# Optimization experiments

Hardware: AMD Instinct MI355X
Metric: run time of the kernel (lower is better)

The kernel has to match this reference:

```python
import jax, jax.numpy as jnp
import numpy as np

D_MODEL = 1024
N_HEAD = 16
D_K = D_MODEL // N_HEAD
B, S = 2, 2048
NEG = -1000000000.0


def setup_inputs() -> dict:
    key = jax.random.key(0)
    ks = jax.random.split(key, 9)
    inp = {
        "input_q": jax.random.normal(ks[0], (B, S, D_MODEL), dtype=jnp.float32),
        "input_k": jax.random.normal(ks[1], (B, S, D_MODEL), dtype=jnp.float32),
        "input_v": jax.random.normal(ks[2], (B, S, D_MODEL), dtype=jnp.float32),
        "mask": jax.random.randint(ks[3], (1, 1, S, S), 0, 2, dtype=jnp.int32),
        # parameters (Linear weights stored as [in, out] for x @ W)
        "w_q": jax.random.normal(ks[4], (D_MODEL, D_MODEL), dtype=jnp.float32) / np.sqrt(D_MODEL),
        "w_k": jax.random.normal(ks[5], (D_MODEL, D_MODEL), dtype=jnp.float32) / np.sqrt(D_MODEL),
        "w_v": jax.random.normal(ks[6], (D_MODEL, D_MODEL), dtype=jnp.float32) / np.sqrt(D_MODEL),
        "w_o": jax.random.normal(ks[7], (D_MODEL, D_MODEL), dtype=jnp.float32) / np.sqrt(D_MODEL),
        "b_o": jax.random.normal(ks[8], (D_MODEL,), dtype=jnp.float32) * 0.01,
    }
    return inp


def reference(input_q, input_k, input_v, mask, w_q, w_k, w_v, w_o, b_o):
    b = input_q.shape[0]
    # QKV projections -> [B, H, S, d_k]
    def split_heads(x):
        return x.reshape(b, -1, N_HEAD, D_K).transpose(0, 2, 1, 3)
    q = split_heads(input_q @ w_q)
    k = split_heads(input_k @ w_k)
    v = split_heads(input_v @ w_v)
    # naive attention: materialize [B, H, Sq, Sk] scores
    scores = jnp.einsum("bhqd,bhkd->bhqk", q, k) / jnp.sqrt(jnp.float32(D_K))
    scores = jnp.where(mask == 0, jnp.float32(NEG), scores)
    attn = jax.nn.softmax(scores, axis=-1)
    per_head = jnp.einsum("bhqk,bhkd->bhqd", attn, v)
    concat = per_head.transpose(0, 2, 1, 3).reshape(b, -1, N_HEAD * D_K)
    return concat @ w_o + b_o
```

## Files before the change

### kernel.cpp

```cpp
#include <hip/hip_runtime.h>
#include <hip/hip_bf16.h>

typedef _Float16 halfx8 __attribute__((ext_vector_type(8)));
typedef _Float16 halfx4 __attribute__((ext_vector_type(4)));
typedef _Float16 half2t __attribute__((ext_vector_type(2)));
typedef __fp16 fp16x2 __attribute__((ext_vector_type(2)));
typedef float floatx4 __attribute__((ext_vector_type(4)));

constexpr int S = 2048;
constexpr int DM = 1024;
constexpr int NH = 16;
constexpr int DK = 64;
constexpr int BATCH = 2;
constexpr int MROWS = 4096;
constexpr float QSCALE = 0.125f * 1.44269504088896340736f;

#if defined(__has_builtin)
#if __has_builtin(__builtin_amdgcn_fdot2)
#define HAVE_FDOT2 1
#endif
#endif

static __device__ inline half2t pack2(float a, float b) {
  return __builtin_bit_cast(half2t, __builtin_amdgcn_cvt_pkrtz(a, b));
}

__global__ void convert_w4(const float* __restrict__ w0, const float* __restrict__ w1,
                           const float* __restrict__ w2, const float* __restrict__ w3,
                           _Float16* __restrict__ o0, _Float16* __restrict__ o1,
                           _Float16* __restrict__ o2, _Float16* __restrict__ o3) {
  const float* w = (blockIdx.z == 0) ? w0 : (blockIdx.z == 1) ? w1 : (blockIdx.z == 2) ? w2 : w3;
  _Float16* wt = (blockIdx.z == 0) ? o0 : (blockIdx.z == 1) ? o1 : (blockIdx.z == 2) ? o2 : o3;
  __shared__ float tile[32][33];
  int n0 = blockIdx.x * 32, k0 = blockIdx.y * 32;
  int tx = threadIdx.x, ty = threadIdx.y;
#pragma unroll
  for (int i = 0; i < 4; ++i)
    tile[ty + i * 8][tx] = w[(k0 + ty + i * 8) * DM + n0 + tx];
  __syncthreads();
#pragma unroll
  for (int i = 0; i < 4; ++i)
    wt[(n0 + ty + i * 8) * DM + k0 + tx] = (_Float16)tile[tx][ty + i * 8];
}

__global__ void convert_in3(const float* __restrict__ a0, const float* __restrict__ a1,
                            const float* __restrict__ a2, _Float16* __restrict__ o0,
                            _Float16* __restrict__ o1, _Float16* __restrict__ o2) {
  const float* a = (blockIdx.z == 0) ? a0 : (blockIdx.z == 1) ? a1 : a2;
  _Float16* o = (blockIdx.z == 0) ? o0 : (blockIdx.z == 1) ? o1 : o2;
  size_t i = ((size_t)blockIdx.x * 256 + threadIdx.x) * 8;
  float4 va = *(const float4*)(a + i);
  float4 vb = *(const float4*)(a + i + 4);
  union { halfx8 v; _Float16 h[8]; } u;
  u.h[0] = (_Float16)va.x; u.h[1] = (_Float16)va.y;
  u.h[2] = (_Float16)va.z; u.h[3] = (_Float16)va.w;
  u.h[4] = (_Float16)vb.x; u.h[5] = (_Float16)vb.y;
  u.h[6] = (_Float16)vb.z; u.h[7] = (_Float16)vb.w;
  *(halfx8*)(o + i) = u.v;
}

__global__ void mask_fp16(const int* __restrict__ m, _Float16* __restrict__ Mh) {
  size_t i = ((size_t)blockIdx.x * 256 + threadIdx.x) * 8;
  int4 a = *(const int4*)(m + i);
  int4 b = *(const int4*)(m + i + 4);
  union { halfx8 v; _Float16 h[8]; } u;
  u.h[0] = (_Float16)(a.x != 0); u.h[1] = (_Float16)(a.y != 0);
  u.h[2] = (_Float16)(a.z != 0); u.h[3] = (_Float16)(a.w != 0);
  u.h[4] = (_Float16)(b.x != 0); u.h[5] = (_Float16)(b.y != 0);
  u.h[6] = (_Float16)(b.z != 0); u.h[7] = (_Float16)(b.w != 0);
  *(halfx8*)(Mh + i) = u.v;
}

__global__ __launch_bounds__(256) void qkv_gemm(const _Float16* __restrict__ xq,
                                                const _Float16* __restrict__ xk,
                                                const _Float16* __restrict__ xv,
                                                const _Float16* __restrict__ wqkv,
                                                _Float16* __restrict__ Qh,
                                                _Float16* __restrict__ Kh,
                                                _Float16* __restrict__ Vt) {
  constexpr int LDT = 72;
  __shared__ __align__(16) _Float16 smem[2 * 128 * LDT];
  _Float16* Asm = smem;
  _Float16* Bsm = smem + 128 * LDT;
  const int tid = threadIdx.x;
  const int w = tid >> 6, l = tid & 63, lo = l & 15, quad = l >> 4;
  const int wm = (w >> 1) * 64, wn = (w & 1) * 64;
  const int bx = blockIdx.x, bm = blockIdx.y * 128;
  const int wid = bx >> 3;
  const _Float16* A = (wid == 0) ? xq : (wid == 1) ? xk : xv;
  const _Float16* Bt = wqkv + (size_t)bx * 128 * DM;

  const int srow = tid >> 1, scol = (tid & 1) * 32;
  const _Float16* Aptr = A + (size_t)(bm + srow) * DM + scol;
  const _Float16* Bptr = Bt + (size_t)srow * DM + scol;

  floatx4 acc[4][4] = {};

  for (int k0 = 0; k0 < DM; k0 += 64) {
#pragma unroll
    for (int i = 0; i < 4; ++i)
      *(halfx8*)&Asm[srow * LDT + scol + i * 8] = *(const halfx8*)(Aptr + k0 + i * 8);
#pragma unroll
    for (int i = 0; i < 4; ++i)
      *(halfx8*)&Bsm[srow * LDT + scol + i * 8] = *(const halfx8*)(Bptr + k0 + i * 8);
    __syncthreads();

#pragma unroll
    for (int ks = 0; ks < 2; ++ks) {
      halfx8 af[4], bf[4];
#pragma unroll
      for (int mt = 0; mt < 4; ++mt)
        af[mt] = *(const halfx8*)&Asm[(wm + mt * 16 + lo) * LDT + ks * 32 + quad * 8];
#pragma unroll
      for (int nt = 0; nt < 4; ++nt)
        bf[nt] = *(const halfx8*)&Bsm[(wn + nt * 16 + lo) * LDT + ks * 32 + quad * 8];
#pragma unroll
      for (int mt = 0; mt < 4; ++mt)
#pragma unroll
        for (int nt = 0; nt < 4; ++nt)
          acc[mt][nt] =
              __builtin_amdgcn_mfma_f32_16x16x32_f16(af[mt], bf[nt], acc[mt][nt], 0, 0, 0);
    }
    __syncthreads();
  }

  if (wid == 2) {
    constexpr int LDTT = 136;
    _Float16* tb = smem;
#pragma unroll
    for (int mt = 0; mt < 4; ++mt)
#pragma unroll
      for (int nt = 0; nt < 4; ++nt)
#pragma unroll
        for (int r = 0; r < 4; ++r) {
          int dl = wn + nt * 16 + lo;
          int sl = wm + mt * 16 + quad * 4 + r;
          tb[dl * LDTT + sl] = (_Float16)acc[mt][nt][r];
        }
    __syncthreads();
    const int b = bm >> 11, s0 = bm & (S - 1);
    const int d2 = tid >> 1, chunk = (tid & 1) * 64;
    const int dg = ((bx & 7) * 128 + d2);
    const int h = dg >> 6, dd = dg & 63;
    _Float16* O = Vt + ((size_t)(b * NH + h) * DK + dd) * S + s0 + chunk;
#pragma unroll
    for (int j = 0; j < 8; ++j)
      *(halfx8*)(O + j * 8) = *(const halfx8*)&tb[d2 * LDTT + chunk + j * 8];
    return;
  }

  _Float16* Out = (wid == 0) ? Qh : Kh;
  const float scale = (wid == 0) ? QSCALE : 1.0f;
#pragma unroll
  for (int mt = 0; mt < 4; ++mt)
#pragma unroll
    for (int nt = 0; nt < 4; ++nt)
#pragma unroll
      for (int r = 0; r < 4; ++r) {
        int row = bm + wm + mt * 16 + quad * 4 + r;
        int n = (bx & 7) * 128 + wn + nt * 16 + lo;
        int b = row >> 11, s = row & (S - 1);
        int h = n >> 6, d = n & 63;
        Out[((size_t)(b * NH + h) * S + s) * DK + d] = (_Float16)(acc[mt][nt][r] * scale);
      }
}

__global__ __launch_bounds__(256) void attn_kernel(const _Float16* __restrict__ Q,
                                                   const _Float16* __restrict__ Kh,
                                                   const _Float16* __restrict__ Vt,
                                                   const _Float16* __restrict__ Mh,
                                                   _Float16* __restrict__ concat) {
  constexpr int LDT = 72;
  __shared__ __align__(16) _Float16 Ksm[64 * LDT];
  __shared__ __align__(16) _Float16 Vsm[64 * LDT];
  __shared__ __align__(16) _Float16 Psm[4 * 16 * LDT];

  const int tid = threadIdx.x;
  const int w = tid >> 6, l = tid & 63, lo = l & 15, quad = l >> 4;
  const int qb = blockIdx.x * 64 + w * 16;
  const int h = blockIdx.y, b = blockIdx.z;

  const _Float16* Qb = Q + (size_t)(b * NH + h) * S * DK;
  const _Float16* Kb = Kh + (size_t)(b * NH + h) * S * DK;
  const _Float16* Vb = Vt + (size_t)(b * NH + h) * DK * S;
  const _Float16* Mq = Mh + (size_t)(qb + lo) * S;

  halfx8 qf[2];
#pragma unroll
  for (int ks = 0; ks < 2; ++ks)
    qf[ks] = *(const halfx8*)(Qb + (qb + lo) * DK + ks * 32 + quad * 8);

  floatx4 Oacc[4] = {};
  float lsum = 0.f;
  const half2t onev = {(_Float16)1.0f, (_Float16)1.0f};

  const int srow = tid >> 2, scol = (tid & 3) * 16;
  const _Float16* Kp = Kb + srow * DK + scol;
  const _Float16* Vp = Vb + srow * S + scol;
  _Float16* Pw = &Psm[w * 16 * LDT];

  for (int kt = 0; kt < S / 64; ++kt) {
#pragma unroll
    for (int i = 0; i < 2; ++i) {
      *(halfx8*)&Ksm[srow * LDT + scol + i * 8] = *(const halfx8*)(Kp + kt * 64 * DK + i * 8);
      *(halfx8*)&Vsm[srow * LDT + scol + i * 8] = *(const halfx8*)(Vp + kt * 64 + i * 8);
    }
    __syncthreads();

    floatx4 Sacc[4] = {};
#pragma unroll
    for (int ks = 0; ks < 2; ++ks)
#pragma unroll
      for (int nt = 0; nt < 4; ++nt) {
        halfx8 kf = *(const halfx8*)&Ksm[(nt * 16 + lo) * LDT + ks * 32 + quad * 8];
        Sacc[nt] = __builtin_amdgcn_mfma_f32_16x16x32_f16(kf, qf[ks], Sacc[nt], 0, 0, 0);
      }

#pragma unroll
    for (int nt = 0; nt < 4; ++nt) {
      union { halfx4 v; half2t h[2]; } mv;
      mv.v = *(const halfx4*)(Mq + kt * 64 + nt * 16 + quad * 4);
      half2t p01 = pack2(__builtin_exp2f(Sacc[nt][0]), __builtin_exp2f(Sacc[nt][1]));
      half2t p23 = pack2(__builtin_exp2f(Sacc[nt][2]), __builtin_exp2f(Sacc[nt][3]));
      p01 *= mv.h[0];
      p23 *= mv.h[1];
#ifdef HAVE_FDOT2
      lsum = __builtin_amdgcn_fdot2(__builtin_bit_cast(fp16x2, p01),
                                    __builtin_bit_cast(fp16x2, onev), lsum, false);
      lsum = __builtin_amdgcn_fdot2(__builtin_bit_cast(fp16x2, p23),
                                    __builtin_bit_cast(fp16x2, onev), lsum, false);
#else
      lsum += (float)p01[0] + (float)p01[1] + (float)p23[0] + (float)p23[1];
#endif
      union { halfx4 v; half2t h[2]; } u;
      u.h[0] = p01; u.h[1] = p23;
      *(halfx4*)&Pw[lo * LDT + nt * 16 + quad * 4] = u.v;
    }

#pragma unroll
    for (int ks = 0; ks < 2; ++ks) {
      halfx8 pf = *(const halfx8*)&Pw[lo * LDT + ks * 32 + quad * 8];
#pragma unroll
      for (int nt = 0; nt < 4; ++nt) {
        halfx8 vf = *(const halfx8*)&Vsm[(nt * 16 + lo) * LDT + ks * 32 + quad * 8];
        Oacc[nt] = __builtin_amdgcn_mfma_f32_16x16x32_f16(pf, vf, Oacc[nt], 0, 0, 0);
      }
    }
    __syncthreads();
  }

  lsum += __shfl_xor(lsum, 16);
  lsum += __shfl_xor(lsum, 32);

#pragma unroll
  for (int r = 0; r < 4; ++r) {
    float lr = __shfl(lsum, quad * 4 + r);
    float inv = __builtin_amdgcn_rcpf(lr);
    int q = qb + quad * 4 + r;
#pragma unroll
    for (int nt = 0; nt < 4; ++nt) {
      int d = nt * 16 + lo;
      concat[((size_t)b * S + q) * DM + h * DK + d] = (_Float16)(Oacc[nt][r] * inv);
    }
  }
}

__global__ __launch_bounds__(256) void out_gemm(const _Float16* __restrict__ A,
                                                const _Float16* __restrict__ Bt,
                                                float* __restrict__ Cp,
                                                const float* __restrict__ bias) {
  constexpr int LDT = 72;
  __shared__ __align__(16) _Float16 Asm[128 * LDT];
  __shared__ __align__(16) _Float16 Bsm[64 * LDT];
  const int tid = threadIdx.x;
  const int w = tid >> 6, l = tid & 63, lo = l & 15, quad = l >> 4;
  const int wm = (w >> 1) * 64, wn = (w & 1) * 32;
  const int bm = blockIdx.y * 128, bn = blockIdx.x * 64;

  const int arow = tid >> 1, acol = (tid & 1) * 32;
  const int brow = tid >> 2, bcol = (tid & 3) * 16;

  floatx4 acc[4][2] = {};

  for (int k0 = 0; k0 < DM; k0 += 64) {
#pragma unroll
    for (int i = 0; i < 4; ++i)
      *(halfx8*)&Asm[arow * LDT + acol + i * 8] =
          *(const halfx8*)(A + (size_t)(bm + arow) * DM + k0 + acol + i * 8);
#pragma unroll
    for (int i = 0; i < 2; ++i)
      *(halfx8*)&Bsm[brow * LDT + bcol + i * 8] =
          *(const halfx8*)(Bt + (size_t)(bn + brow) * DM + k0 + bcol + i * 8);
    __syncthreads();

#pragma unroll
    for (int ks = 0; ks < 2; ++ks) {
      halfx8 af[4], bfr[2];
#pragma unroll
      for (int mt = 0; mt < 4; ++mt)
        af[mt] = *(const halfx8*)&Asm[(wm + mt * 16 + lo) * LDT + ks * 32 + quad * 8];
#pragma unroll
      for (int nt = 0; nt < 2; ++nt)
        bfr[nt] = *(const halfx8*)&Bsm[(wn + nt * 16 + lo) * LDT + ks * 32 + quad * 8];
#pragma unroll
      for (int mt = 0; mt < 4; ++mt)
#pragma unroll
        for (int nt = 0; nt < 2; ++nt)
          acc[mt][nt] =
              __builtin_amdgcn_mfma_f32_16x16x32_f16(af[mt], bfr[nt], acc[mt][nt], 0, 0, 0);
    }
    __syncthreads();
  }

#pragma unroll
  for (int mt = 0; mt < 4; ++mt)
#pragma unroll
    for (int nt = 0; nt < 2; ++nt)
#pragma unroll
      for (int r = 0; r < 4; ++r) {
        int row = bm + wm + mt * 16 + quad * 4 + r;
        int col = bn + wn + nt * 16 + lo;
        Cp[(size_t)row * DM + col] = acc[mt][nt][r] + bias[col];
      }
}

extern "C" void kernel_launch(void* const* d_in, const int* in_sizes, int n_in,
                              void* d_out, int out_size, void* d_ws, size_t ws_size,
                              hipStream_t stream) {
  const float* in_q = (const float*)d_in[0];
  const float* in_k = (const float*)d_in[1];
  const float* in_v = (const float*)d_in[2];
  const int* mask = (const int*)d_in[3];
  const float* w_q = (const float*)d_in[4];
  const float* w_k = (const float*)d_in[5];
  const float* w_v = (const float*)d_in[6];
  const float* w_o = (const float*)d_in[7];
  const float* b_o = (const float*)d_in[8];
  float* out = (float*)d_out;

  char* ws = (char*)d_ws;
  constexpr size_t WB = (size_t)DM * DM * sizeof(_Float16);
  constexpr size_t MB_ = (size_t)S * S * sizeof(_Float16);
  constexpr size_t TB = (size_t)MROWS * DM * sizeof(_Float16);
  _Float16* wqkv = (_Float16*)(ws);
  _Float16* wto = (_Float16*)(ws + 3 * WB);
  _Float16* Mh = (_Float16*)(ws + 4 * WB);
  char* p = ws + 4 * WB + MB_;
  _Float16* Qh = (_Float16*)(p);
  _Float16* Kh = (_Float16*)(p + TB);
  _Float16* Vt = (_Float16*)(p + 2 * TB);
  _Float16* xq = (_Float16*)(p + 3 * TB);
  _Float16* xk = (_Float16*)(p + 4 * TB);
  _Float16* xv = (_Float16*)(p + 5 * TB);
  _Float16* concat = xq;

  convert_w4<<<dim3(32, 32, 4), dim3(32, 8), 0, stream>>>(
      w_q, w_k, w_v, w_o, wqkv, wqkv + DM * DM, wqkv + 2 * DM * DM, wto);
  convert_in3<<<dim3(MROWS * DM / 8 / 256, 1, 3), 256, 0, stream>>>(in_q, in_k, in_v,
                                                                    xq, xk, xv);
  mask_fp16<<<dim3(S * S / 8 / 256), 256, 0, stream>>>(mask, Mh);

  qkv_gemm<<<dim3(24, 32), 256, 0, stream>>>(xq, xk, xv, wqkv, Qh, Kh, Vt);
  attn_kernel<<<dim3(S / 64, NH, BATCH), 256, 0, stream>>>(Qh, Kh, Vt, Mh, concat);
  out_gemm<<<dim3(DM / 64, MROWS / 128), 256, 0, stream>>>(concat, wto, out, b_o);
}
```

Measured before the change: 293.7 us.

## Use direct global-to-LDS loads with XOR-swizzled tiles and pre-swizzled mask layout

All three matmul-style kernels now stage tiles with global_load_lds (16-byte direct-to-LDS loads) into unpadded 64-wide tiles that use an XOR swizzle to avoid bank conflicts, in place of register round-trips into padded LDS. Q and K are stored row-major as [B*S, DM] instead of per-head layouts, which simplifies the GEMM epilogue. The mask is pre-rearranged into a per-tile, per-lane order so each lane fetches its 16 mask values with two 16-byte loads issued before the barrier. This reduces VGPR traffic and load latency, at the cost of a more complex addressing scheme and reliance on the direct-LDS builtin's placement semantics.

```diff
diff --git a/kernel.cpp b/kernel.cpp
--- a/kernel.cpp
+++ b/kernel.cpp
@@ -23,6 +23,11 @@
 
 static __device__ inline half2t pack2(float a, float b) {
   return __builtin_bit_cast(half2t, __builtin_amdgcn_cvt_pkrtz(a, b));
+}
+
+static __device__ inline void load_lds16(const _Float16* g, _Float16* l) {
+  __builtin_amdgcn_global_load_lds((const __attribute__((address_space(1))) void*)g,
+                                   (__attribute__((address_space(3))) void*)l, 16, 0, 0);
 }
 
 __global__ void convert_w4(const float* __restrict__ w0, const float* __restrict__ w1,
@@ -59,50 +64,59 @@
   *(halfx8*)(o + i) = u.v;
 }
 
-__global__ void mask_fp16(const int* __restrict__ m, _Float16* __restrict__ Mh) {
-  size_t i = ((size_t)blockIdx.x * 256 + threadIdx.x) * 8;
-  int4 a = *(const int4*)(m + i);
-  int4 b = *(const int4*)(m + i + 4);
+__global__ void mask_swz(const int* __restrict__ m, _Float16* __restrict__ Mt) {
+  int t = blockIdx.x * 256 + threadIdx.x;
+  int j0 = (t & 1) * 8;
+  int quad = (t >> 1) & 3;
+  int q = (t >> 3) & (S - 1);
+  int kt = t >> 14;
+  const int* src = m + (size_t)q * S + kt * 64 + (j0 >> 2) * 16 + quad * 4;
+  int4 a = *(const int4*)src;
+  int4 b = *(const int4*)(src + 16);
   union { halfx8 v; _Float16 h[8]; } u;
   u.h[0] = (_Float16)(a.x != 0); u.h[1] = (_Float16)(a.y != 0);
   u.h[2] = (_Float16)(a.z != 0); u.h[3] = (_Float16)(a.w != 0);
   u.h[4] = (_Float16)(b.x != 0); u.h[5] = (_Float16)(b.y != 0);
   u.h[6] = (_Float16)(b.z != 0); u.h[7] = (_Float16)(b.w != 0);
-  *(halfx8*)(Mh + i) = u.v;
+  *(halfx8*)(Mt + (size_t)t * 8) = u.v;
 }
 
 __global__ __launch_bounds__(256) void qkv_gemm(const _Float16* __restrict__ xq,
                                                 const _Float16* __restrict__ xk,
                                                 const _Float16* __restrict__ xv,
                                                 const _Float16* __restrict__ wqkv,
-                                                _Float16* __restrict__ Qh,
-                                                _Float16* __restrict__ Kh,
+                                                _Float16* __restrict__ Qf,
+                                                _Float16* __restrict__ Kf,
                                                 _Float16* __restrict__ Vt) {
-  constexpr int LDT = 72;
-  __shared__ __align__(16) _Float16 smem[2 * 128 * LDT];
+  __shared__ __align__(16) _Float16 smem[17408];
   _Float16* Asm = smem;
-  _Float16* Bsm = smem + 128 * LDT;
+  _Float16* Bsm = smem + 128 * 64;
   const int tid = threadIdx.x;
   const int w = tid >> 6, l = tid & 63, lo = l & 15, quad = l >> 4;
+  const int lo7 = l & 7;
   const int wm = (w >> 1) * 64, wn = (w & 1) * 64;
   const int bx = blockIdx.x, bm = blockIdx.y * 128;
   const int wid = bx >> 3;
   const _Float16* A = (wid == 0) ? xq : (wid == 1) ? xk : xv;
   const _Float16* Bt = wqkv + (size_t)bx * 128 * DM;
 
-  const int srow = tid >> 1, scol = (tid & 1) * 32;
-  const _Float16* Aptr = A + (size_t)(bm + srow) * DM + scol;
-  const _Float16* Bptr = Bt + (size_t)srow * DM + scol;
-
   floatx4 acc[4][4] = {};
 
   for (int k0 = 0; k0 < DM; k0 += 64) {
 #pragma unroll
-    for (int i = 0; i < 4; ++i)
-      *(halfx8*)&Asm[srow * LDT + scol + i * 8] = *(const halfx8*)(Aptr + k0 + i * 8);
-#pragma unroll
-    for (int i = 0; i < 4; ++i)
-      *(halfx8*)&Bsm[srow * LDT + scol + i * 8] = *(const halfx8*)(Bptr + k0 + i * 8);
+    for (int i = 0; i < 4; ++i) {
+      int chunk = i * 256 + tid;
+      int r = chunk >> 3;
+      int c = (chunk & 7) ^ (r & 7);
+      load_lds16(A + (size_t)(bm + r) * DM + k0 + c * 8, Asm + chunk * 8);
+    }
+#pragma unroll
+    for (int i = 0; i < 4; ++i) {
+      int chunk = i * 256 + tid;
+      int r = chunk >> 3;
+      int c = (chunk & 7) ^ (r & 7);
+      load_lds16(Bt + (size_t)r * DM + k0 + c * 8, Bsm + chunk * 8);
+    }
     __syncthreads();
 
 #pragma unroll
@@ -110,10 +124,10 @@
       halfx8 af[4], bf[4];
 #pragma unroll
       for (int mt = 0; mt < 4; ++mt)
-        af[mt] = *(const halfx8*)&Asm[(wm + mt * 16 + lo) * LDT + ks * 32 + quad * 8];
+        af[mt] = *(const halfx8*)&Asm[(wm + mt * 16 + lo) * 64 + (((ks * 4 + quad) ^ lo7) * 8)];
 #pragma unroll
       for (int nt = 0; nt < 4; ++nt)
-        bf[nt] = *(const halfx8*)&Bsm[(wn + nt * 16 + lo) * LDT + ks * 32 + quad * 8];
+        bf[nt] = *(const halfx8*)&Bsm[(wn + nt * 16 + lo) * 64 + (((ks * 4 + quad) ^ lo7) * 8)];
 #pragma unroll
       for (int mt = 0; mt < 4; ++mt)
 #pragma unroll
@@ -149,7 +163,7 @@
     return;
   }
 
-  _Float16* Out = (wid == 0) ? Qh : Kh;
+  _Float16* Out = (wid == 0) ? Qf : Kf;
   const float scale = (wid == 0) ? QSCALE : 1.0f;
 #pragma unroll
   for (int mt = 0; mt < 4; ++mt)
@@ -158,53 +172,51 @@
 #pragma unroll
       for (int r = 0; r < 4; ++r) {
         int row = bm + wm + mt * 16 + quad * 4 + r;
-        int n = (bx & 7) * 128 + wn + nt * 16 + lo;
-        int b = row >> 11, s = row & (S - 1);
-        int h = n >> 6, d = n & 63;
-        Out[((size_t)(b * NH + h) * S + s) * DK + d] = (_Float16)(acc[mt][nt][r] * scale);
+        int col = (bx & 7) * 128 + wn + nt * 16 + lo;
+        Out[(size_t)row * DM + col] = (_Float16)(acc[mt][nt][r] * scale);
       }
 }
 
-__global__ __launch_bounds__(256) void attn_kernel(const _Float16* __restrict__ Q,
-                                                   const _Float16* __restrict__ Kh,
+__global__ __launch_bounds__(256) void attn_kernel(const _Float16* __restrict__ Qf,
+                                                   const _Float16* __restrict__ Kf,
                                                    const _Float16* __restrict__ Vt,
-                                                   const _Float16* __restrict__ Mh,
+                                                   const _Float16* __restrict__ Mt,
                                                    _Float16* __restrict__ concat) {
-  constexpr int LDT = 72;
-  __shared__ __align__(16) _Float16 Ksm[64 * LDT];
-  __shared__ __align__(16) _Float16 Vsm[64 * LDT];
-  __shared__ __align__(16) _Float16 Psm[4 * 16 * LDT];
+  __shared__ __align__(16) _Float16 Ksm[64 * 64];
+  __shared__ __align__(16) _Float16 Vsm[64 * 64];
+  __shared__ __align__(16) _Float16 Psm[4 * 16 * 64];
 
   const int tid = threadIdx.x;
   const int w = tid >> 6, l = tid & 63, lo = l & 15, quad = l >> 4;
+  const int lo7 = l & 7;
   const int qb = blockIdx.x * 64 + w * 16;
   const int h = blockIdx.y, b = blockIdx.z;
 
-  const _Float16* Qb = Q + (size_t)(b * NH + h) * S * DK;
-  const _Float16* Kb = Kh + (size_t)(b * NH + h) * S * DK;
   const _Float16* Vb = Vt + (size_t)(b * NH + h) * DK * S;
-  const _Float16* Mq = Mh + (size_t)(qb + lo) * S;
+  const _Float16* Mw = Mt + ((size_t)(qb + lo) * 4 + quad) * 16;
 
   halfx8 qf[2];
 #pragma unroll
   for (int ks = 0; ks < 2; ++ks)
-    qf[ks] = *(const halfx8*)(Qb + (qb + lo) * DK + ks * 32 + quad * 8);
+    qf[ks] = *(const halfx8*)(Qf + ((size_t)b * S + qb + lo) * DM + h * DK + ks * 32 + quad * 8);
 
   floatx4 Oacc[4] = {};
   float lsum = 0.f;
   const half2t onev = {(_Float16)1.0f, (_Float16)1.0f};
-
-  const int srow = tid >> 2, scol = (tid & 3) * 16;
-  const _Float16* Kp = Kb + srow * DK + scol;
-  const _Float16* Vp = Vb + srow * S + scol;
-  _Float16* Pw = &Psm[w * 16 * LDT];
+  _Float16* Pw = &Psm[w * 16 * 64];
 
   for (int kt = 0; kt < S / 64; ++kt) {
 #pragma unroll
     for (int i = 0; i < 2; ++i) {
-      *(halfx8*)&Ksm[srow * LDT + scol + i * 8] = *(const halfx8*)(Kp + kt * 64 * DK + i * 8);
-      *(halfx8*)&Vsm[srow * LDT + scol + i * 8] = *(const halfx8*)(Vp + kt * 64 + i * 8);
-    }
+      int chunk = i * 256 + tid;
+      int r = chunk >> 3;
+      int c = (chunk & 7) ^ (r & 7);
+      load_lds16(Kf + ((size_t)b * S + kt * 64 + r) * DM + h * DK + c * 8, Ksm + chunk * 8);
+      load_lds16(Vb + (size_t)r * S + kt * 64 + c * 8, Vsm + chunk * 8);
+    }
+    union { halfx8 v; half2t h2[4]; } m0, m1;
+    m0.v = *(const halfx8*)(Mw + (size_t)kt * 131072);
+    m1.v = *(const halfx8*)(Mw + (size_t)kt * 131072 + 8);
     __syncthreads();
 
     floatx4 Sacc[4] = {};
@@ -212,18 +224,19 @@
     for (int ks = 0; ks < 2; ++ks)
 #pragma unroll
       for (int nt = 0; nt < 4; ++nt) {
-        halfx8 kf = *(const halfx8*)&Ksm[(nt * 16 + lo) * LDT + ks * 32 + quad * 8];
+        halfx8 kf = *(const halfx8*)&Ksm[(nt * 16 + lo) * 64 + (((ks * 4 + quad) ^ lo7) * 8)];
         Sacc[nt] = __builtin_amdgcn_mfma_f32_16x16x32_f16(kf, qf[ks], Sacc[nt], 0, 0, 0);
       }
 
+    half2t mm[8];
+    mm[0] = m0.h2[0]; mm[1] = m0.h2[1]; mm[2] = m0.h2[2]; mm[3] = m0.h2[3];
+    mm[4] = m1.h2[0]; mm[5] = m1.h2[1]; mm[6] = m1.h2[2]; mm[7] = m1.h2[3];
 #pragma unroll
     for (int nt = 0; nt < 4; ++nt) {
-      union { halfx4 v; half2t h[2]; } mv;
-      mv.v = *(const halfx4*)(Mq + kt * 64 + nt * 16 + quad * 4);
       half2t p01 = pack2(__builtin_exp2f(Sacc[nt][0]), __builtin_exp2f(Sacc[nt][1]));
       half2t p23 = pack2(__builtin_exp2f(Sacc[nt][2]), __builtin_exp2f(Sacc[nt][3]));
-      p01 *= mv.h[0];
-      p23 *= mv.h[1];
+      p01 *= mm[nt * 2];
+      p23 *= mm[nt * 2 + 1];
 #ifdef HAVE_FDOT2
       lsum = __builtin_amdgcn_fdot2(__builtin_bit_cast(fp16x2, p01),
                                     __builtin_bit_cast(fp16x2, onev), lsum, false);
@@ -234,15 +247,15 @@
 #endif
       union { halfx4 v; half2t h[2]; } u;
       u.h[0] = p01; u.h[1] = p23;
-      *(halfx4*)&Pw[lo * LDT + nt * 16 + quad * 4] = u.v;
+      *(halfx4*)&Pw[lo * 64 + (((2 * nt + (quad >> 1)) ^ lo7) * 8) + (quad & 1) * 4] = u.v;
     }
 
 #pragma unroll
     for (int ks = 0; ks < 2; ++ks) {
-      halfx8 pf = *(const halfx8*)&Pw[lo * LDT + ks * 32 + quad * 8];
+      halfx8 pf = *(const halfx8*)&Pw[lo * 64 + (((ks * 4 + quad) ^ lo7) * 8)];
 #pragma unroll
       for (int nt = 0; nt < 4; ++nt) {
-        halfx8 vf = *(const halfx8*)&Vsm[(nt * 16 + lo) * LDT + ks * 32 + quad * 8];
+        halfx8 vf = *(const halfx8*)&Vsm[(nt * 16 + lo) * 64 + (((ks * 4 + quad) ^ lo7) * 8)];
         Oacc[nt] = __builtin_amdgcn_mfma_f32_16x16x32_f16(pf, vf, Oacc[nt], 0, 0, 0);
       }
     }
@@ -269,28 +282,31 @@
                                                 const _Float16* __restrict__ Bt,
                                                 float* __restrict__ Cp,
                                                 const float* __restrict__ bias) {
-  constexpr int LDT = 72;
-  __shared__ __align__(16) _Float16 Asm[128 * LDT];
-  __shared__ __align__(16) _Float16 Bsm[64 * LDT];
+  __shared__ __align__(16) _Float16 Asm[128 * 64];
+  __shared__ __align__(16) _Float16 Bsm[64 * 64];
   const int tid = threadIdx.x;
   const int w = tid >> 6, l = tid & 63, lo = l & 15, quad = l >> 4;
+  const int lo7 = l & 7;
   const int wm = (w >> 1) * 64, wn = (w & 1) * 32;
   const int bm = blockIdx.y * 128, bn = blockIdx.x * 64;
 
-  const int arow = tid >> 1, acol = (tid & 1) * 32;
-  const int brow = tid >> 2, bcol = (tid & 3) * 16;
-
   floatx4 acc[4][2] = {};
 
   for (int k0 = 0; k0 < DM; k0 += 64) {
 #pragma unroll
-    for (int i = 0; i < 4; ++i)
-      *(halfx8*)&Asm[arow * LDT + acol + i * 8] =
-          *(const halfx8*)(A + (size_t)(bm + arow) * DM + k0 + acol + i * 8);
-#pragma unroll
-    for (int i = 0; i < 2; ++i)
-      *(halfx8*)&Bsm[brow * LDT + bcol + i * 8] =
-          *(const halfx8*)(Bt + (size_t)(bn + brow) * DM + k0 + bcol + i * 8);
+    for (int i = 0; i < 4; ++i) {
+      int chunk = i * 256 + tid;
+      int r = chunk >> 3;
+      int c = (chunk & 7) ^ (r & 7);
+      load_lds16(A + (size_t)(bm + r) * DM + k0 + c * 8, Asm + chunk * 8);
+    }
+#pragma unroll
+    for (int i = 0; i < 2; ++i) {
+      int chunk = i * 256 + tid;
+      int r = chunk >> 3;
+      int c = (chunk & 7) ^ (r & 7);
+      load_lds16(Bt + (size_t)(bn + r) * DM + k0 + c * 8, Bsm + chunk * 8);
+    }
     __syncthreads();
 
 #pragma unroll
@@ -298,10 +314,10 @@
       halfx8 af[4], bfr[2];
 #pragma unroll
       for (int mt = 0; mt < 4; ++mt)
-        af[mt] = *(const halfx8*)&Asm[(wm + mt * 16 + lo) * LDT + ks * 32 + quad * 8];
+        af[mt] = *(const halfx8*)&Asm[(wm + mt * 16 + lo) * 64 + (((ks * 4 + quad) ^ lo7) * 8)];
 #pragma unroll
       for (int nt = 0; nt < 2; ++nt)
-        bfr[nt] = *(const halfx8*)&Bsm[(wn + nt * 16 + lo) * LDT + ks * 32 + quad * 8];
+        bfr[nt] = *(const halfx8*)&Bsm[(wn + nt * 16 + lo) * 64 + (((ks * 4 + quad) ^ lo7) * 8)];
 #pragma unroll
       for (int mt = 0; mt < 4; ++mt)
 #pragma unroll
@@ -344,10 +360,10 @@
   constexpr size_t TB = (size_t)MROWS * DM * sizeof(_Float16);
   _Float16* wqkv = (_Float16*)(ws);
   _Float16* wto = (_Float16*)(ws + 3 * WB);
-  _Float16* Mh = (_Float16*)(ws + 4 * WB);
+  _Float16* Mt = (_Float16*)(ws + 4 * WB);
   char* p = ws + 4 * WB + MB_;
-  _Float16* Qh = (_Float16*)(p);
-  _Float16* Kh = (_Float16*)(p + TB);
+  _Float16* Qf = (_Float16*)(p);
+  _Float16* Kf = (_Float16*)(p + TB);
   _Float16* Vt = (_Float16*)(p + 2 * TB);
   _Float16* xq = (_Float16*)(p + 3 * TB);
   _Float16* xk = (_Float16*)(p + 4 * TB);
@@ -358,9 +374,9 @@
       w_q, w_k, w_v, w_o, wqkv, wqkv + DM * DM, wqkv + 2 * DM * DM, wto);
   convert_in3<<<dim3(MROWS * DM / 8 / 256, 1, 3), 256, 0, stream>>>(in_q, in_k, in_v,
                                                                     xq, xk, xv);
-  mask_fp16<<<dim3(S * S / 8 / 256), 256, 0, stream>>>(mask, Mh);
-
-  qkv_gemm<<<dim3(24, 32), 256, 0, stream>>>(xq, xk, xv, wqkv, Qh, Kh, Vt);
-  attn_kernel<<<dim3(S / 64, NH, BATCH), 256, 0, stream>>>(Qh, Kh, Vt, Mh, concat);
+  mask_swz<<<dim3(S * S / 8 / 256), 256, 0, stream>>>(mask, Mt);
+
+  qkv_gemm<<<dim3(24, 32), 256, 0, stream>>>(xq, xk, xv, wqkv, Qf, Kf, Vt);
+  attn_kernel<<<dim3(S / 64, NH, BATCH), 256, 0, stream>>>(Qf, Kf, Vt, Mt, concat);
   out_gemm<<<dim3(DM / 64, MROWS / 128), 256, 0, stream>>>(concat, wto, out, b_o);
 }
```

Measured after the change: 266.3 us. 9.3% less time.
